# Performance work log

Hardware: AMD Instinct MI355X
Metric: run time of the kernel (lower is better)

## Reference

```python
import jax, jax.numpy as jnp
import numpy as np

N_FILTERS = 256
N_ITER = 10
N_HISTORY = 5
N_CLASSES = 1000
N_BITS = 8
# pool_strategy=[3] -> pool when t % 3 == 2
POOL = [(t % 3 == 2) for t in range(N_ITER)]
EPS = 1e-5


def quantifier(w, n_bit=N_BITS):
    # Faithful to source: maxWeight returns 0 if max|w| < 1 else -1 (while loop runs <= once),
    # then divide -> int truncation -> divide.
    m = jnp.where(jnp.max(jnp.abs(w)) < 1.0, 0.0, -1.0).astype(w.dtype)
    v = jnp.exp2(jnp.asarray(n_bit - 1, w.dtype) + m)
    return jnp.trunc(w / v) / v


def conv3x3(x, w):
    # NCHW, OIHW, stride 1, padding 1 (same)
    return jax.lax.conv_general_dilated(
        x, w, window_strides=(1, 1), padding=((1, 1), (1, 1)),
        dimension_numbers=("NCHW", "OIHW", "NCHW"))


def maxpool2(x):
    n, c, h, w = x.shape
    return jnp.max(x.reshape(n, c, h // 2, 2, w // 2, 2), axis=(3, 5))


def batchnorm(a, gamma, beta):
    # training-mode BN: batch statistics over (N, H, W), biased variance, eps=1e-5
    mu = jnp.mean(a, axis=(0, 2, 3), keepdims=True)
    var = jnp.var(a, axis=(0, 2, 3), keepdims=True)
    xhat = (a - mu) * jax.lax.rsqrt(var + EPS)
    return gamma[None, :, None, None] * xhat + beta[None, :, None, None]


def setup_inputs() -> dict:
    key = jax.random.key(0)
    ks = jax.random.split(key, 7)
    SCALE = 200.0  # scale so the truncation quantizer (v=64 when max>=1) yields nonzero levels
    x = jax.random.normal(ks[0], (32, 3, 64, 64), jnp.float32) * SCALE
    # quantize() is applied to params at init in the torch module -> pre-quantize here
    conv_w = quantifier(jax.random.normal(ks[1], (N_FILTERS, N_FILTERS, 3, 3), jnp.float32) * SCALE)
    lin_w = quantifier(jax.random.normal(ks[2], (N_CLASSES, N_FILTERS), jnp.float32) * SCALE)
    lin_b = quantifier(jax.random.normal(ks[3], (N_CLASSES,), jnp.float32) * SCALE)
    alpha = quantifier(jax.random.normal(ks[4], (N_ITER, N_HISTORY + 1), jnp.float32) * SCALE)
    bn_gamma = jax.random.uniform(ks[5], (N_ITER, N_FILTERS), jnp.float32, 64.0, 256.0)
    bn_beta = jax.random.normal(ks[6], (N_ITER, N_FILTERS), jnp.float32)
    return dict(x=x, conv_w=conv_w, lin_w=lin_w, lin_b=lin_b, alpha=alpha,
                bn_gamma=bn_gamma, bn_beta=bn_beta)


def reference(x, conv_w, lin_w, lin_b, alpha, bn_gamma, bn_beta):
    # pad channels 3 -> N_FILTERS, then fake-quantize activations
    x0 = quantifier(jnp.pad(x, ((0, 0), (0, N_FILTERS - x.shape[1]), (0, 0), (0, 0))))
    # faithful: hist[0] is never written by the source's shift loop, stays None
    hist = [None] * (N_HISTORY - 1) + [x0]
    for t in range(N_ITER):
        a = alpha[t, 0] * jax.nn.relu(conv3x3(hist[-1], conv_w))
        for i, h in enumerate(hist):
            if h is not None:
                a = a + alpha[t, i + 1] * h
        a = quantifier(batchnorm(a, bn_gamma[t], bn_beta[t]))
        for i in range(1, N_HISTORY - 1):
            hist[i] = hist[i + 1]
        hist[N_HISTORY - 1] = a
        if POOL[t]:
            hist = [None if h is None else maxpool2(h) for h in hist]
    feat = jnp.max(hist[-1], axis=(2, 3))  # adaptive_max_pool2d to (1,1)
    return feat @ lin_w.T + lin_b
```

## Files before the change

kernel.cpp:

```cpp
#include <hip/hip_runtime.h>
#include <hip/hip_bf16.h>


typedef unsigned short u16;
typedef signed char i8;
typedef unsigned long long ull;
typedef long long ll;
typedef int i32x4 __attribute__((ext_vector_type(4)));

__device__ __forceinline__ void glds16(const i8* g, i8* l) {
    __builtin_amdgcn_global_load_lds(
        (const __attribute__((address_space(1))) void*)g,
        (__attribute__((address_space(3))) void*)l, 16, 0, 0);
}

__global__ void fill_kernel(float* __restrict__ out, int n, float v) {
    int i = blockIdx.x * 256 + threadIdx.x;
    if (i < n) out[i] = v;
}

__global__ void wt_kernel(const float* __restrict__ w, i8* __restrict__ wt) {
    int g = blockIdx.x * 256 + threadIdx.x;
    int base = g * 16;
    int ci0 = base & 255;
    int co  = (base >> 8) & 255;
    int tap = base >> 16;
    i8 tmp[16];
#pragma unroll
    for (int j = 0; j < 16; j++)
        tmp[j] = (i8)__builtin_rintf(w[((co << 8) + ci0 + j) * 9 + tap] * 64.0f);
    *(uint4*)(wt + base) = *(const uint4*)tmp;
}

__global__ void qx_kernel(const float* __restrict__ x, i8* __restrict__ out) {
    int g = blockIdx.x * 256 + threadIdx.x;
    int chunk = g & 15;
    int p = g >> 4;
    i8 tmp[16];
#pragma unroll
    for (int j = 0; j < 16; j++) tmp[j] = 0;
    if (chunk == 0) {
        int n  = p / 4356;
        int pp = p - n * 4356;
        int py = pp / 66;
        int px = pp - py * 66;
        if (py >= 1 && py <= 64 && px >= 1 && px <= 64) {
            int yx = ((py - 1) << 6) + (px - 1);
#pragma unroll
            for (int c = 0; c < 3; c++)
                tmp[c] = (i8)truncf(x[((n * 3 + c) << 12) + yx] * (1.0f / 64.0f));
        }
    }
    *(uint4*)(out + (size_t)g * 16) = *(const uint4*)tmp;
}

__global__ void stats_init(ull* s1, ull* s2, int* kmn, int* kmx) {
    int i = blockIdx.x * 256 + threadIdx.x;
    s1[i] = 0ull; s2[i] = 0ull;
    kmn[i] = 0x7fffffff; kmx[i] = -0x7fffffff - 1;
}

template<int NH>
__global__ __launch_bounds__(256) void conv_kernel(
    const i8* __restrict__ act, const i8* __restrict__ wtp, int* __restrict__ a_pre,
    const i8* __restrict__ h0, const i8* __restrict__ h1,
    const i8* __restrict__ h2, const i8* __restrict__ h3,
    const float* __restrict__ alphas, int t,
    int W, int logW, int PW, int nA,
    ull* __restrict__ s1g, ull* __restrict__ s2g,
    int* __restrict__ kmng, int* __restrict__ kmxg)
{
    __shared__ __align__(16) i8 As[320 * 64];
    __shared__ __align__(16) i8 Bs[3 * 128 * 64];
    const int tid  = threadIdx.x;
    const int G    = gridDim.x;
    const int d    = blockIdx.x;
    const int sw   = (d & 7) * (G >> 3) + (d >> 3);
    const int m0   = (sw >> 1) * 128;
    const int c0   = (sw & 1) * 128;
    const int lane = tid & 63;
    const int wv   = tid >> 6;
    const int wm   = (wv & 1) * 64;
    const int wn   = (wv >> 1) * 64;
    const int l15  = lane & 15;
    const int quad = lane >> 4;
    const int logHW = 2 * logW;
    const int HW   = W * W;
    const int PP   = PW * PW;

    i32x4 acc[4][4];
#pragma unroll
    for (int i = 0; i < 4; i++)
#pragma unroll
        for (int j = 0; j < 4; j++) acc[i][j] = (i32x4){0, 0, 0, 0};

    const int n0 = m0 >> logHW;
    const int y0 = (m0 & (HW - 1)) >> logW;
    const long bandstart = (long)n0 * PP + (long)y0 * PW;

    int pb[4];
#pragma unroll
    for (int i = 0; i < 4; i++) {
        int mr = m0 + wm + i * 16 + l15;
        int nn = mr >> logHW;
        int rr = mr & (HW - 1);
        pb[i] = (nn - n0) * PP + ((rr >> logW) - y0 + 1) * PW + (rr & (W - 1)) + 1;
    }

    const int qrow = tid >> 2;
    const int bb   = (tid & 3) * 16;
    i8* const ldsbaseA = As + wv * 1024 + lane * 16;
    const int ko = quad * 16;

    for (int chunk = 0; chunk < 4; ++chunk) {
        const int cb = chunk * 64;
#pragma unroll
        for (int g = 0; g < 3; ++g) {
            __syncthreads();
            if (g == 0) {
                for (int k = 0; k < nA; ++k)
                    glds16(act + (bandstart + qrow + k * 64) * 256 + cb + bb,
                           ldsbaseA + k * 4096);
            }
#pragma unroll
            for (int tt = 0; tt < 3; ++tt) {
                const int tap = 3 * g + tt;
#pragma unroll
                for (int p = 0; p < 2; ++p)
                    glds16(wtp + (tap << 16) + ((c0 + qrow + p * 64) << 8) + cb + bb,
                           Bs + tt * 8192 + wv * 1024 + p * 4096 + lane * 16);
            }
            __syncthreads();
#pragma unroll
            for (int tt = 0; tt < 3; ++tt) {
                const int tap = 3 * g + tt;
                const int dY  = tap / 3 - 1;
                const int dX  = tap % 3 - 1;
                const int uoff = dY * PW + dX;
                i32x4 bf[4];
#pragma unroll
                for (int j = 0; j < 4; j++)
                    bf[j] = *(const i32x4*)(&Bs[tt * 8192 + (wn + j * 16 + l15) * 64 + ko]);
#pragma unroll
                for (int i = 0; i < 4; i++) {
                    i32x4 af = *(const i32x4*)(&As[(pb[i] + uoff) * 64 + ko]);
#pragma unroll
                    for (int j = 0; j < 4; j++)
                        acc[i][j] = __builtin_amdgcn_mfma_i32_16x16x64_i8(af, bf[j], acc[i][j], 0, 0, 0);
                }
            }
        }
    }

    const int a0k = (int)__builtin_rintf(alphas[t * 6] * 64.0f);
    int aq64[NH];
    const i8* hp[4] = {h0, h1, h2, h3};
#pragma unroll
    for (int q = 0; q < NH; q++)
        aq64[q] = (int)__builtin_rintf(alphas[t * 6 + (6 - NH) + q] * 64.0f) * 64;

    const int shard = sw & 15;
#pragma unroll
    for (int j = 0; j < 4; j++) {
        const int cg = c0 + wn + j * 16 + l15;
        ll s1 = 0, s2 = 0;
        int mn = 0x7fffffff, mx = -0x7fffffff - 1;
#pragma unroll
        for (int i = 0; i < 4; i++) {
            const int mo0 = m0 + wm + i * 16 + quad * 4;
            const int n   = mo0 >> logHW;
            const int rem = mo0 & (HW - 1);
            const int yy  = rem >> logW;
            const int xx  = rem & (W - 1);
            const int phb = (((n * PW + yy + 1) * PW) + xx + 1) << 8;
#pragma unroll
            for (int r = 0; r < 4; r++) {
                const int idx  = ((mo0 + r) << 8) + cg;
                const int pidx = phb + (r << 8) + cg;
                int K = acc[i][j][r];
                int av = a0k * (K > 0 ? K : 0);
#pragma unroll
                for (int q = 0; q < NH; q++) av += aq64[q] * (int)hp[q][pidx];
                a_pre[idx] = av;
                s1 += av;
                s2 += (ll)av * (ll)av;
                mn = av < mn ? av : mn;
                mx = av > mx ? av : mx;
            }
        }
        s1 += __shfl_xor(s1, 16); s1 += __shfl_xor(s1, 32);
        s2 += __shfl_xor(s2, 16); s2 += __shfl_xor(s2, 32);
        int o;
        o = __shfl_xor(mn, 16); mn = o < mn ? o : mn;
        o = __shfl_xor(mn, 32); mn = o < mn ? o : mn;
        o = __shfl_xor(mx, 16); mx = o > mx ? o : mx;
        o = __shfl_xor(mx, 32); mx = o > mx ? o : mx;
        if (quad == 0) {
            const int sidx = shard * 2560 + t * 256 + cg;
            atomicAdd(&s1g[sidx], (ull)s1);
            atomicAdd(&s2g[sidx], (ull)s2);
            atomicMin(&kmng[sidx], mn);
            atomicMax(&kmxg[sidx], mx);
        }
    }
}

__global__ void finalize_kernel(const ull* __restrict__ s1g, const ull* __restrict__ s2g,
                                const int* __restrict__ kmng, const int* __restrict__ kmxg,
                                const float* __restrict__ g1, const float* __restrict__ g2,
                                int t, int M, double* mu_o, double* rs_o, float* invv) {
    __shared__ float red[256];
    int c = threadIdx.x;
    const float* G = (g1[0] >= 32.0f) ? g1 : g2;
    const float* B = (g1[0] >= 32.0f) ? g2 : g1;
    ll S1i = 0, S2i = 0;
    int kmn = 0x7fffffff, kmx = -0x7fffffff - 1;
    for (int sh = 0; sh < 16; sh++) {
        int sidx = sh * 2560 + t * 256 + c;
        S1i += (ll)s1g[sidx];
        S2i += (ll)s2g[sidx];
        int a = kmng[sidx]; kmn = a < kmn ? a : kmn;
        int b2 = kmxg[sidx]; kmx = b2 > kmx ? b2 : kmx;
    }
    double S1 = (double)S1i;
    double S2 = (double)S2i;
    double Md = (double)M;
    double mu = S1 / (Md * 262144.0);
    double var = (S2 - S1 * S1 / Md) / (Md * 68719476736.0);
    if (var < 0.0) var = 0.0;
    double rs = 1.0 / sqrt(var + 1e-5);
    mu_o[c] = mu; rs_o[c] = rs;
    double g = (double)G[t * 256 + c];
    double b = (double)B[t * 256 + c];
    double lo = (double)kmn * (1.0 / 262144.0);
    double hi = (double)kmx * (1.0 / 262144.0);
    double bnlo = g * ((lo - mu) * rs) + b;
    double bnhi = g * ((hi - mu) * rs) + b;
    red[c] = (float)fmax(fabs(bnlo), fabs(bnhi));
    __syncthreads();
    for (int s = 128; s > 0; s >>= 1) {
        if (c < s) red[c] = fmaxf(red[c], red[c + s]);
        __syncthreads();
    }
    if (c == 0) invv[0] = (red[0] < 1.0f) ? (1.0f / 128.0f) : (1.0f / 64.0f);
}

__global__ void bnq_kernel(const int* __restrict__ a, i8* __restrict__ out,
                           const double* __restrict__ mu, const double* __restrict__ rs,
                           const float* __restrict__ g1, const float* __restrict__ g2,
                           int t, const float* __restrict__ invv,
                           int W, int logW, int PW) {
    int c = threadIdx.x;
    int sp = blockIdx.x;
    int PP = PW * PW;
    int n  = sp / PP;
    int pp = sp - n * PP;
    int py = pp / PW;
    int px = pp - py * PW;
    int y = py - 1, x = px - 1;
    i8 v = 0;
    if ((unsigned)y < (unsigned)W && (unsigned)x < (unsigned)W) {
        const float* G = (g1[0] >= 32.0f) ? g1 : g2;
        const float* B = (g1[0] >= 32.0f) ? g2 : g1;
        double m = mu[c], r = rs[c];
        double g = (double)G[t * 256 + c];
        double b = (double)B[t * 256 + c];
        double iv = (double)invv[0];
        int idx = (((n << logW) + y) << logW << 8) + (x << 8) + c;
        double bn = g * (((double)a[idx] * (1.0 / 262144.0) - m) * r) + b;
        v = (i8)(int)trunc(bn * iv);
    }
    out[((size_t)sp << 8) + c] = v;
}

__global__ void bnqpool_kernel(const int* __restrict__ a, i8* __restrict__ out,
                               const double* __restrict__ mu, const double* __restrict__ rs,
                               const float* __restrict__ g1, const float* __restrict__ g2,
                               int t, const float* __restrict__ invv, int Dout) {
    int c = threadIdx.x;
    int sp = blockIdx.x;
    int P = Dout + 2;
    int PP = P * P;
    int n  = sp / PP;
    int pp = sp - n * PP;
    int py = pp / P;
    int px = pp - py * P;
    int y = py - 1, x = px - 1;
    i8 v = 0;
    if ((unsigned)y < (unsigned)Dout && (unsigned)x < (unsigned)Dout) {
        const float* G = (g1[0] >= 32.0f) ? g1 : g2;
        const float* B = (g1[0] >= 32.0f) ? g2 : g1;
        double m = mu[c], r = rs[c];
        double g = (double)G[t * 256 + c];
        double b = (double)B[t * 256 + c];
        double iv = (double)invv[0];
        int Din = Dout << 1;
        int ib = (((n * Din + 2 * y) * Din) + 2 * x) << 8;
        int rowstr = Din << 8;
        int k0 = a[ib + c], k1 = a[ib + 256 + c];
        int k2 = a[ib + rowstr + c], k3 = a[ib + rowstr + 256 + c];
        int km = k0 > k1 ? k0 : k1;
        if (k2 > km) km = k2;
        if (k3 > km) km = k3;
        double bn = g * (((double)km * (1.0 / 262144.0) - m) * r) + b;
        v = (i8)(int)trunc(bn * iv);
    }
    out[((size_t)sp << 8) + c] = v;
}

__global__ void pool_kernel(const i8* __restrict__ in, i8* __restrict__ out, int Dout) {
    int c = threadIdx.x;
    int sp = blockIdx.x;
    int P = Dout + 2;
    int PP = P * P;
    int n  = sp / PP;
    int pp = sp - n * PP;
    int py = pp / P;
    int px = pp - py * P;
    int y = py - 1, x = px - 1;
    i8 v = 0;
    if ((unsigned)y < (unsigned)Dout && (unsigned)x < (unsigned)Dout) {
        int PIN = 2 * Dout + 2;
        int ib = ((n * PIN + 2 * y + 1) * PIN + 2 * x + 1) << 8;
        int rowstr = PIN << 8;
        int a0 = in[ib + c], a1 = in[ib + 256 + c];
        int a2 = in[ib + rowstr + c], a3 = in[ib + rowstr + 256 + c];
        int m = a0 > a1 ? a0 : a1;
        if (a2 > m) m = a2;
        if (a3 > m) m = a3;
        v = (i8)m;
    }
    out[((size_t)sp << 8) + c] = v;
}

__global__ void featlin_kernel(const i8* __restrict__ a9, const float* __restrict__ lw,
                               const float* __restrict__ lb, float* __restrict__ out) {
    __shared__ float fsh[256];
    int n = blockIdx.x, c = threadIdx.x;
    int mx = -1000;
    for (int r = 0; r < 64; r++) {
        int y = r >> 3, x = r & 7;
        int v = a9[(((n * 100 + (y + 1) * 10 + x + 1)) << 8) + c];
        if (v > mx) mx = v;
    }
    fsh[c] = (float)mx * (1.0f / 64.0f);
    __syncthreads();
    for (int k = c; k < 1000; k += 256) {
        float acc = lb[k];
        const float* wr = lw + k * 256;
        for (int cc = 0; cc < 256; cc++) acc = fmaf(fsh[cc], wr[cc], acc);
        out[n * 1000 + k] = acc;
    }
}

extern "C" void kernel_launch(void* const* d_in, const int* in_sizes, int n_in,
                              void* d_out, int out_size, void* d_ws, size_t ws_size,
                              hipStream_t stream) {
    const float *xin = 0, *conv_w = 0, *lin_w = 0, *lin_b = 0, *alphas = 0, *gb1 = 0, *gb2 = 0;
    for (int i = 0; i < n_in; i++) {
        const float* p = (const float*)d_in[i];
        switch (in_sizes[i]) {
            case 393216: xin = p; break;
            case 589824: conv_w = p; break;
            case 256000: lin_w = p; break;
            case 1000:   lin_b = p; break;
            case 60:     alphas = p; break;
            case 2560:   if (!gb1) gb1 = p; else gb2 = p; break;
            default: break;
        }
    }

    char* ws = (char*)d_ws;
    const size_t FRSZ = 35684352ull;
    const size_t SSSZ = 9469952ull;
    i8* FR[3];
    for (int i = 0; i < 3; i++) FR[i] = (i8*)(ws + (size_t)i * FRSZ);
    char* AP = ws + 3 * FRSZ;
    int* a_pre = (int*)AP;
    i8* SS[7];
    for (int i = 0; i < 6; i++) SS[i] = (i8*)(AP + 33554432ull + (size_t)i * SSSZ);
    SS[6] = (i8*)(ws + 3 * FRSZ + 134217728ull);
    i8* wt = (i8*)((char*)SS[6] + SSSZ);
    size_t off = (size_t)(((char*)wt - ws)) + 589824ull;
    ull*    s1g  = (ull*)(ws + off);    off += 327680;
    ull*    s2g  = (ull*)(ws + off);    off += 327680;
    int*    kmng = (int*)(ws + off);    off += 163840;
    int*    kmxg = (int*)(ws + off);    off += 163840;
    double* mu   = (double*)(ws + off); off += 2048;
    double* rs   = (double*)(ws + off); off += 2048;
    float*  invv = (float*)(ws + off);  off += 256;
    const size_t need = off;

    if (!xin || !conv_w || !lin_w || !lin_b || !alphas || !gb1 || !gb2) {
        fill_kernel<<<(out_size + 255) / 256, 256, 0, stream>>>((float*)d_out, out_size, 1792.0f);
        return;
    }
    if (ws_size < need) {
        float sv = 1000.0f + (float)(ws_size >> 20);
        fill_kernel<<<(out_size + 255) / 256, 256, 0, stream>>>((float*)d_out, out_size, sv);
        return;
    }

    wt_kernel<<<144, 256, 0, stream>>>(conv_w, wt);
    qx_kernel<<<8712, 256, 0, stream>>>(xin, FR[0]);
    stats_init<<<160, 256, 0, stream>>>(s1g, s2g, kmng, kmxg);

    auto conv_part = [&](int t, int D, i8* actp, i8* p0, i8* p1, i8* p2, i8* p3, int nh) {
        int logW = __builtin_ctz(D);
        int M = 32 * D * D;
        int G = (M / 128) * 2;
        int nA = (D == 64) ? 5 : (D == 16 ? 3 : 4);
        switch (nh) {
            case 1: conv_kernel<1><<<G, 256, 0, stream>>>(actp, wt, a_pre, p0, p1, p2, p3,
                        alphas, t, D, logW, D + 2, nA, s1g, s2g, kmng, kmxg); break;
            case 2: conv_kernel<2><<<G, 256, 0, stream>>>(actp, wt, a_pre, p0, p1, p2, p3,
                        alphas, t, D, logW, D + 2, nA, s1g, s2g, kmng, kmxg); break;
            case 3: conv_kernel<3><<<G, 256, 0, stream>>>(actp, wt, a_pre, p0, p1, p2, p3,
                        alphas, t, D, logW, D + 2, nA, s1g, s2g, kmng, kmxg); break;
            default: conv_kernel<4><<<G, 256, 0, stream>>>(actp, wt, a_pre, p0, p1, p2, p3,
                        alphas, t, D, logW, D + 2, nA, s1g, s2g, kmng, kmxg); break;
        }
        finalize_kernel<<<1, 256, 0, stream>>>(s1g, s2g, kmng, kmxg, gb1, gb2, t, M, mu, rs, invv);
    };
    auto bnq_part = [&](int t, int D, i8* outp) {
        int PW = D + 2;
        bnq_kernel<<<32 * PW * PW, 256, 0, stream>>>(a_pre, outp, mu, rs, gb1, gb2, t, invv,
                                                     D, __builtin_ctz(D), PW);
    };
    auto bnqpool_part = [&](int t, int Dout, i8* outp) {
        int P = Dout + 2;
        bnqpool_kernel<<<32 * P * P, 256, 0, stream>>>(a_pre, outp, mu, rs, gb1, gb2, t, invv, Dout);
    };
    auto pool_part = [&](int Dout, i8* inp, i8* outp) {
        int P = Dout + 2;
        pool_kernel<<<32 * P * P, 256, 0, stream>>>(inp, outp, Dout);
    };

    conv_part(0, 64, FR[0], FR[0], FR[0], FR[0], FR[0], 1);
    bnq_part(0, 64, FR[1]);
    conv_part(1, 64, FR[1], FR[0], FR[1], FR[1], FR[1], 2);
    bnq_part(1, 64, FR[2]);
    conv_part(2, 64, FR[2], FR[0], FR[1], FR[2], FR[2], 3);
    bnqpool_part(2, 32, SS[6]);
    pool_part(32, FR[0], SS[0]);
    pool_part(32, FR[1], SS[1]);
    pool_part(32, FR[2], SS[2]);
    conv_part(3, 32, SS[6], SS[0], SS[1], SS[2], SS[6], 4);
    bnq_part(3, 32, SS[3]);
    conv_part(4, 32, SS[3], SS[1], SS[2], SS[6], SS[3], 4);
    bnq_part(4, 32, SS[4]);
    conv_part(5, 32, SS[4], SS[2], SS[6], SS[3], SS[4], 4);
    bnqpool_part(5, 16, SS[5]);
    pool_part(16, SS[6], SS[0]);
    pool_part(16, SS[3], SS[1]);
    pool_part(16, SS[4], SS[2]);
    conv_part(6, 16, SS[5], SS[0], SS[1], SS[2], SS[5], 4);
    bnq_part(6, 16, SS[3]);
    conv_part(7, 16, SS[3], SS[1], SS[2], SS[5], SS[3], 4);
    bnq_part(7, 16, SS[4]);
    conv_part(8, 16, SS[4], SS[2], SS[5], SS[3], SS[4], 4);
    bnqpool_part(8, 8, SS[6]);
    pool_part(8, SS[5], SS[0]);
    pool_part(8, SS[3], SS[1]);
    pool_part(8, SS[4], SS[2]);
    conv_part(9, 8, SS[6], SS[0], SS[1], SS[2], SS[6], 4);
    bnq_part(9, 8, SS[3]);

    featlin_kernel<<<32, 256, 0, stream>>>(SS[3], lin_w, lin_b, (float*)d_out);
}
```

Before: 1.042 ms.

## Double-buffer weight tiles in LDS to overlap loads with MFMA compute

Flattens the chunk/group loop into 12 steps and double-buffers the B (weight) LDS tile, so the next step's weight load is issued before the current step's MFMAs run. This replaces two barriers per step with one and hides global-to-LDS latency for the weights. The activation tile is still single-buffered, so its reload costs an extra barrier every three steps. Doubling the B buffer raises LDS use, which may lower occupancy.

```diff
diff --git a/kernel.cpp b/kernel.cpp
--- a/kernel.cpp
+++ b/kernel.cpp
@@ -71,7 +71,7 @@
     int* __restrict__ kmng, int* __restrict__ kmxg)
 {
     __shared__ __align__(16) i8 As[320 * 64];
-    __shared__ __align__(16) i8 Bs[3 * 128 * 64];
+    __shared__ __align__(16) i8 Bs[2 * 3 * 128 * 64];
     const int tid  = threadIdx.x;
     const int G    = gridDim.x;
     const int d    = blockIdx.x;
@@ -109,46 +109,62 @@
 
     const int qrow = tid >> 2;
     const int bb   = (tid & 3) * 16;
-    i8* const ldsbaseA = As + wv * 1024 + lane * 16;
+    const int lane16 = lane * 16;
+    i8* const ldsbaseA = As + wv * 1024 + lane16;
     const int ko = quad * 16;
 
-    for (int chunk = 0; chunk < 4; ++chunk) {
-        const int cb = chunk * 64;
-#pragma unroll
-        for (int g = 0; g < 3; ++g) {
-            __syncthreads();
-            if (g == 0) {
-                for (int k = 0; k < nA; ++k)
-                    glds16(act + (bandstart + qrow + k * 64) * 256 + cb + bb,
-                           ldsbaseA + k * 4096);
+    auto stageA = [&](int cb) {
+        for (int k = 0; k < nA; ++k)
+            glds16(act + (bandstart + qrow + k * 64) * 256 + cb + bb,
+                   ldsbaseA + k * 4096);
+    };
+    auto stageB = [&](int w1) {
+        const int ch1 = (w1 * 11) >> 5;
+        const int g1  = w1 - 3 * ch1;
+        const int cb1 = ch1 * 64;
+        i8* const bdst = Bs + (w1 & 1) * 24576 + wv * 1024 + lane16;
+#pragma unroll
+        for (int tt = 0; tt < 3; ++tt) {
+            const int tap = 3 * g1 + tt;
+#pragma unroll
+            for (int p = 0; p < 2; ++p)
+                glds16(wtp + (tap << 16) + ((c0 + qrow + p * 64) << 8) + cb1 + bb,
+                       bdst + tt * 8192 + p * 4096);
+        }
+    };
+
+    stageA(0);
+    stageB(0);
+    __syncthreads();
+
+    int ch = 0, g = 0;
+    for (int w = 0; w < 12; ++w) {
+        if (w + 1 < 12) stageB(w + 1);
+        const i8* const bsrc = Bs + (w & 1) * 24576;
+#pragma unroll
+        for (int tt = 0; tt < 3; ++tt) {
+            const int uoff = (g - 1) * PW + (tt - 1);
+            i32x4 bf[4];
+#pragma unroll
+            for (int j = 0; j < 4; j++)
+                bf[j] = *(const i32x4*)(&bsrc[tt * 8192 + (wn + j * 16 + l15) * 64 + ko]);
+#pragma unroll
+            for (int i = 0; i < 4; i++) {
+                i32x4 af = *(const i32x4*)(&As[(pb[i] + uoff) * 64 + ko]);
+#pragma unroll
+                for (int j = 0; j < 4; j++)
+                    acc[i][j] = __builtin_amdgcn_mfma_i32_16x16x64_i8(af, bf[j], acc[i][j], 0, 0, 0);
             }
-#pragma unroll
-            for (int tt = 0; tt < 3; ++tt) {
-                const int tap = 3 * g + tt;
-#pragma unroll
-                for (int p = 0; p < 2; ++p)
-                    glds16(wtp + (tap << 16) + ((c0 + qrow + p * 64) << 8) + cb + bb,
-                           Bs + tt * 8192 + wv * 1024 + p * 4096 + lane * 16);
+        }
+        __syncthreads();
+        if (g == 2) {
+            if (w + 1 < 12) {
+                stageA((ch + 1) * 64);
+                __syncthreads();
             }
-            __syncthreads();
-#pragma unroll
-            for (int tt = 0; tt < 3; ++tt) {
-                const int tap = 3 * g + tt;
-                const int dY  = tap / 3 - 1;
-                const int dX  = tap % 3 - 1;
-                const int uoff = dY * PW + dX;
-                i32x4 bf[4];
-#pragma unroll
-                for (int j = 0; j < 4; j++)
-                    bf[j] = *(const i32x4*)(&Bs[tt * 8192 + (wn + j * 16 + l15) * 64 + ko]);
-#pragma unroll
-                for (int i = 0; i < 4; i++) {
-                    i32x4 af = *(const i32x4*)(&As[(pb[i] + uoff) * 64 + ko]);
-#pragma unroll
-                    for (int j = 0; j < 4; j++)
-                        acc[i][j] = __builtin_amdgcn_mfma_i32_16x16x64_i8(af, bf[j], acc[i][j], 0, 0, 0);
-                }
-            }
+            ch += 1; g = 0;
+        } else {
+            g += 1;
         }
     }
 
```

After: 1.044 ms. No clear change (+0.2%).
